# Kernel optimization log

Measured on AMD Instinct MI355X. Metric: run time of the kernel, lower is better.

Reference implementation:

```python
import jax, jax.numpy as jnp
import numpy as np

TAU_MEM = 0.005   # sinabs LIF tau_mem (in time-step units)
THR = 1.0         # default spike_threshold
BATCH = 16        # LIFSqueeze batch_size; leading dim is BATCH * T
BETA = 10.0       # surrogate gradient sharpness (sinabs SingleExponential default)


@jax.custom_vjp
def spike_fn(v):
    # MultiSpike: number of spikes = floor(v / thr), clipped at 0
    return jnp.floor(jnp.clip(v / THR, 0.0, None))

def _spike_fwd(v):
    return spike_fn(v), v

def _spike_bwd(v, g):
    # single-exponential surrogate gradient around threshold
    return (g * jnp.exp(-BETA * jnp.abs(v - THR)),)

spike_fn.defvjp(_spike_fwd, _spike_bwd)


def lif(x, spiking=True):
    """LIFSqueeze: x is (BATCH*T, ...); unfold time, scan LIF dynamics, refold."""
    alpha = jnp.exp(jnp.asarray(-1.0 / TAU_MEM, x.dtype))
    T = x.shape[0] // BATCH
    xt = jnp.swapaxes(x.reshape(BATCH, T, *x.shape[1:]), 0, 1)  # (T, B, ...)

    def step(v, xin):
        v = alpha * v + (1.0 - alpha) * xin  # norm_input=True: decay + scaled input
        if spiking:
            s = spike_fn(v)
            return v - s * THR, s            # membrane-subtract reset
        return v, v                          # spike_fn=None -> leaky integrator readout

    _, out = jax.lax.scan(step, jnp.zeros_like(xt[0]), xt)
    return jnp.swapaxes(out, 0, 1).reshape(x.shape)


def conv(x, w, stride, pad):
    return jax.lax.conv_general_dilated(
        x, w, (stride, stride), [(pad, pad), (pad, pad)],
        dimension_numbers=("NCHW", "OIHW", "NCHW"))


def maxpool2(x):
    return jax.lax.reduce_window(x, -jnp.inf, jax.lax.max,
                                 (1, 1, 2, 2), (1, 1, 2, 2), "VALID")


def setup_inputs() -> dict:
    key = jax.random.key(0)
    k = jax.random.split(key, 5)
    x = jax.random.normal(k[0], (1024, 2, 128, 128), jnp.float32)  # (B*T, C, H, W)
    w1 = jax.random.normal(k[1], (8, 2, 2, 2), jnp.float32) * (1.0 / np.sqrt(2 * 4))
    w2 = jax.random.normal(k[2], (8, 8, 3, 3), jnp.float32) * (1.0 / np.sqrt(8 * 9))
    w3 = jax.random.normal(k[3], (8, 8, 3, 3), jnp.float32) * (1.0 / np.sqrt(8 * 9))
    w_fc = jax.random.normal(k[4], (2, 512), jnp.float32) * (1.0 / np.sqrt(512))
    return {"x": x, "w1": w1, "w2": w2, "w3": w3, "w_fc": w_fc}


def reference(x, w1, w2, w3, w_fc):
    h = lif(conv(x, w1, 2, 0))        # (N, 8, 64, 64)
    h = maxpool2(h)                   # (N, 8, 32, 32)
    h = lif(conv(h, w2, 1, 1))
    h = maxpool2(h)                   # (N, 8, 16, 16)
    h = lif(conv(h, w3, 1, 1))
    h = maxpool2(h)                   # (N, 8, 8, 8)
    h = h.reshape(h.shape[0], -1)     # (N, 512)
    h = h @ w_fc.T                    # (N, 2)
    return lif(h, spiking=False)      # membrane-potential readout
```

## Files before the change

### kernel.cpp

```cpp
#include <hip/hip_runtime.h>
#include <cstddef>


__global__ __launch_bounds__(256) void k1_conv_pool(
    const float* __restrict__ x,
    const float* __restrict__ w1,
    float* __restrict__ out)
{
    int idx = blockIdx.x * 256 + threadIdx.x;
    int n  = idx >> 10;
    int py = (idx >> 5) & 31;
    int px = idx & 31;

    float w[64];
#pragma unroll
    for (int i = 0; i < 64; ++i) w[i] = w1[i];

    const float* xb = x + (size_t)n * (2 * 128 * 128);
    float p[2][4][4];
#pragma unroll
    for (int c = 0; c < 2; ++c)
#pragma unroll
        for (int r = 0; r < 4; ++r) {
            float4 v = *reinterpret_cast<const float4*>(
                xb + (c * 128 + 4 * py + r) * 128 + 4 * px);
            p[c][r][0] = v.x; p[c][r][1] = v.y; p[c][r][2] = v.z; p[c][r][3] = v.w;
        }

    float res[8];
#pragma unroll
    for (int co = 0; co < 8; ++co) res[co] = 0.f;

#pragma unroll
    for (int oy = 0; oy < 2; ++oy)
#pragma unroll
    for (int ox = 0; ox < 2; ++ox)
#pragma unroll
    for (int co = 0; co < 8; ++co) {
        float a = 0.f;
#pragma unroll
        for (int c = 0; c < 2; ++c)
#pragma unroll
        for (int kh = 0; kh < 2; ++kh)
#pragma unroll
        for (int kw = 0; kw < 2; ++kw)
            a += p[c][2 * oy + kh][2 * ox + kw] * w[((co * 2 + c) * 2 + kh) * 2 + kw];
        res[co] = fmaxf(res[co], floorf(fmaxf(a, 0.f)));
    }

    float* ob = out + (size_t)n * 8192 + py * 32 + px;
#pragma unroll
    for (int co = 0; co < 8; ++co) ob[co * 1024] = res[co];
}

__global__ __launch_bounds__(256) void k2_conv_pool(
    const float* __restrict__ in,
    const float* __restrict__ w2,
    float* __restrict__ out)
{
    __shared__ float tile[8][34][34];
    int n = blockIdx.x;
    int t = threadIdx.x;

    for (int i = t; i < 8 * 34 * 34; i += 256) (&tile[0][0][0])[i] = 0.f;
    __syncthreads();

    const float4* ib4 = reinterpret_cast<const float4*>(in + (size_t)n * 8192);
    for (int i4 = t; i4 < 2048; i4 += 256) {
        float4 v = ib4[i4];
        int ci = i4 >> 8, y = (i4 >> 3) & 31, x4 = (i4 & 7) << 2;
        tile[ci][y + 1][x4 + 1] = v.x;
        tile[ci][y + 1][x4 + 2] = v.y;
        tile[ci][y + 1][x4 + 3] = v.z;
        tile[ci][y + 1][x4 + 4] = v.w;
    }
    __syncthreads();

    int px = t & 15, py = t >> 4;
    float acc[8][2][2];
#pragma unroll
    for (int i = 0; i < 32; ++i) (&acc[0][0][0])[i] = 0.f;

    for (int ci = 0; ci < 8; ++ci) {
        float p[4][4];
#pragma unroll
        for (int r = 0; r < 4; ++r)
#pragma unroll
            for (int j = 0; j < 4; ++j)
                p[r][j] = tile[ci][2 * py + r][2 * px + j];
#pragma unroll
        for (int co = 0; co < 8; ++co) {
            const float* wp = w2 + (co * 8 + ci) * 9;
            float wv[9];
#pragma unroll
            for (int i = 0; i < 9; ++i) wv[i] = wp[i];
#pragma unroll
            for (int oy = 0; oy < 2; ++oy)
#pragma unroll
            for (int ox = 0; ox < 2; ++ox) {
                float a = acc[co][oy][ox];
#pragma unroll
                for (int kh = 0; kh < 3; ++kh)
#pragma unroll
                for (int kw = 0; kw < 3; ++kw)
                    a += p[oy + kh][ox + kw] * wv[kh * 3 + kw];
                acc[co][oy][ox] = a;
            }
        }
    }

    float* ob = out + (size_t)n * 2048;
#pragma unroll
    for (int co = 0; co < 8; ++co) {
        float m = 0.f;
#pragma unroll
        for (int oy = 0; oy < 2; ++oy)
#pragma unroll
        for (int ox = 0; ox < 2; ++ox)
            m = fmaxf(m, floorf(fmaxf(acc[co][oy][ox], 0.f)));
        ob[co * 256 + t] = m;
    }
}

__global__ __launch_bounds__(256) void k3_conv_pool_fc(
    const float* __restrict__ in,
    const float* __restrict__ w3,
    const float* __restrict__ wfc,
    float* __restrict__ out)
{
    __shared__ float tile[4][8][18][18];
    int t = threadIdx.x;

    for (int i = t; i < 4 * 8 * 18 * 18; i += 256) (&tile[0][0][0][0])[i] = 0.f;
    __syncthreads();

    const float4* ib4 = reinterpret_cast<const float4*>(in) + (size_t)blockIdx.x * 2048;
    for (int i4 = t; i4 < 2048; i4 += 256) {
        float4 v = ib4[i4];
        int sub = i4 >> 9, rem = i4 & 511;
        int ci = rem >> 6, y = (rem >> 2) & 15, x4 = (rem & 3) << 2;
        tile[sub][ci][y + 1][x4 + 1] = v.x;
        tile[sub][ci][y + 1][x4 + 2] = v.y;
        tile[sub][ci][y + 1][x4 + 3] = v.z;
        tile[sub][ci][y + 1][x4 + 4] = v.w;
    }
    __syncthreads();

    int sub = t >> 6;
    int l   = t & 63;
    int py = l >> 3, px = l & 7;

    float acc[8][2][2];
#pragma unroll
    for (int i = 0; i < 32; ++i) (&acc[0][0][0])[i] = 0.f;

    for (int ci = 0; ci < 8; ++ci) {
        float p[4][4];
#pragma unroll
        for (int r = 0; r < 4; ++r)
#pragma unroll
            for (int j = 0; j < 4; ++j)
                p[r][j] = tile[sub][ci][2 * py + r][2 * px + j];
#pragma unroll
        for (int co = 0; co < 8; ++co) {
            const float* wp = w3 + (co * 8 + ci) * 9;
            float wv[9];
#pragma unroll
            for (int i = 0; i < 9; ++i) wv[i] = wp[i];
#pragma unroll
            for (int oy = 0; oy < 2; ++oy)
#pragma unroll
            for (int ox = 0; ox < 2; ++ox) {
                float a = acc[co][oy][ox];
#pragma unroll
                for (int kh = 0; kh < 3; ++kh)
#pragma unroll
                for (int kw = 0; kw < 3; ++kw)
                    a += p[oy + kh][ox + kw] * wv[kh * 3 + kw];
                acc[co][oy][ox] = a;
            }
        }
    }

    float p0 = 0.f, p1 = 0.f;
#pragma unroll
    for (int co = 0; co < 8; ++co) {
        float m = 0.f;
#pragma unroll
        for (int oy = 0; oy < 2; ++oy)
#pragma unroll
        for (int ox = 0; ox < 2; ++ox)
            m = fmaxf(m, floorf(fmaxf(acc[co][oy][ox], 0.f)));
        int o = co * 64 + l;
        p0 += m * wfc[o];
        p1 += m * wfc[512 + o];
    }

#pragma unroll
    for (int off = 32; off > 0; off >>= 1) {
        p0 += __shfl_down(p0, off);
        p1 += __shfl_down(p1, off);
    }
    if (l == 0) {
        int n = blockIdx.x * 4 + sub;
        out[n * 2 + 0] = p0;
        out[n * 2 + 1] = p1;
    }
}

extern "C" void kernel_launch(void* const* d_in, const int* in_sizes, int n_in,
                              void* d_out, int out_size, void* d_ws, size_t ws_size,
                              hipStream_t stream) {
    const float* x   = (const float*)d_in[0];
    const float* w1  = (const float*)d_in[1];
    const float* w2  = (const float*)d_in[2];
    const float* w3  = (const float*)d_in[3];
    const float* wfc = (const float*)d_in[4];
    float* outp = (float*)d_out;

    float* h1 = (float*)d_ws;
    float* h2 = h1 + (size_t)1024 * 8192;

    k1_conv_pool<<<4096, 256, 0, stream>>>(x, w1, h1);
    k2_conv_pool<<<1024, 256, 0, stream>>>(h1, w2, h2);
    k3_conv_pool_fc<<<256, 256, 0, stream>>>(h2, w3, wfc, outp);
}
```

Baseline: 224.5 us.

## Fuse three conv-pool stages into a single per-sample kernel using LDS

Replaces three separate kernels with one kernel in which each block handles one sample. The conv1 and conv2 outputs are kept in shared-memory tiles, so the two intermediate buffers no longer make a round trip through global memory, and two launches go away. The third stage now splits output channels across the four waves, and a shared-memory reduction combines the FC partial sums. The trade-off is higher LDS use per block, which may lower occupancy, and a serialized load-then-compute phase inside each block.

```diff
diff --git a/kernel.cpp b/kernel.cpp
--- a/kernel.cpp
+++ b/kernel.cpp
@@ -2,209 +2,180 @@
 #include <cstddef>
 
 
-__global__ __launch_bounds__(256) void k1_conv_pool(
+__global__ __launch_bounds__(256, 4) void fused_snn(
     const float* __restrict__ x,
     const float* __restrict__ w1,
-    float* __restrict__ out)
-{
-    int idx = blockIdx.x * 256 + threadIdx.x;
-    int n  = idx >> 10;
-    int py = (idx >> 5) & 31;
-    int px = idx & 31;
-
-    float w[64];
-#pragma unroll
-    for (int i = 0; i < 64; ++i) w[i] = w1[i];
-
-    const float* xb = x + (size_t)n * (2 * 128 * 128);
-    float p[2][4][4];
-#pragma unroll
-    for (int c = 0; c < 2; ++c)
-#pragma unroll
-        for (int r = 0; r < 4; ++r) {
-            float4 v = *reinterpret_cast<const float4*>(
-                xb + (c * 128 + 4 * py + r) * 128 + 4 * px);
-            p[c][r][0] = v.x; p[c][r][1] = v.y; p[c][r][2] = v.z; p[c][r][3] = v.w;
-        }
-
-    float res[8];
-#pragma unroll
-    for (int co = 0; co < 8; ++co) res[co] = 0.f;
-
-#pragma unroll
-    for (int oy = 0; oy < 2; ++oy)
-#pragma unroll
-    for (int ox = 0; ox < 2; ++ox)
-#pragma unroll
-    for (int co = 0; co < 8; ++co) {
-        float a = 0.f;
-#pragma unroll
-        for (int c = 0; c < 2; ++c)
-#pragma unroll
-        for (int kh = 0; kh < 2; ++kh)
-#pragma unroll
-        for (int kw = 0; kw < 2; ++kw)
-            a += p[c][2 * oy + kh][2 * ox + kw] * w[((co * 2 + c) * 2 + kh) * 2 + kw];
-        res[co] = fmaxf(res[co], floorf(fmaxf(a, 0.f)));
-    }
-
-    float* ob = out + (size_t)n * 8192 + py * 32 + px;
-#pragma unroll
-    for (int co = 0; co < 8; ++co) ob[co * 1024] = res[co];
-}
-
-__global__ __launch_bounds__(256) void k2_conv_pool(
-    const float* __restrict__ in,
     const float* __restrict__ w2,
-    float* __restrict__ out)
-{
-    __shared__ float tile[8][34][34];
-    int n = blockIdx.x;
-    int t = threadIdx.x;
-
-    for (int i = t; i < 8 * 34 * 34; i += 256) (&tile[0][0][0])[i] = 0.f;
-    __syncthreads();
-
-    const float4* ib4 = reinterpret_cast<const float4*>(in + (size_t)n * 8192);
-    for (int i4 = t; i4 < 2048; i4 += 256) {
-        float4 v = ib4[i4];
-        int ci = i4 >> 8, y = (i4 >> 3) & 31, x4 = (i4 & 7) << 2;
-        tile[ci][y + 1][x4 + 1] = v.x;
-        tile[ci][y + 1][x4 + 2] = v.y;
-        tile[ci][y + 1][x4 + 3] = v.z;
-        tile[ci][y + 1][x4 + 4] = v.w;
-    }
-    __syncthreads();
-
-    int px = t & 15, py = t >> 4;
-    float acc[8][2][2];
-#pragma unroll
-    for (int i = 0; i < 32; ++i) (&acc[0][0][0])[i] = 0.f;
-
-    for (int ci = 0; ci < 8; ++ci) {
-        float p[4][4];
-#pragma unroll
-        for (int r = 0; r < 4; ++r)
-#pragma unroll
-            for (int j = 0; j < 4; ++j)
-                p[r][j] = tile[ci][2 * py + r][2 * px + j];
-#pragma unroll
-        for (int co = 0; co < 8; ++co) {
-            const float* wp = w2 + (co * 8 + ci) * 9;
-            float wv[9];
-#pragma unroll
-            for (int i = 0; i < 9; ++i) wv[i] = wp[i];
-#pragma unroll
-            for (int oy = 0; oy < 2; ++oy)
-#pragma unroll
-            for (int ox = 0; ox < 2; ++ox) {
-                float a = acc[co][oy][ox];
-#pragma unroll
-                for (int kh = 0; kh < 3; ++kh)
-#pragma unroll
-                for (int kw = 0; kw < 3; ++kw)
-                    a += p[oy + kh][ox + kw] * wv[kh * 3 + kw];
-                acc[co][oy][ox] = a;
-            }
-        }
-    }
-
-    float* ob = out + (size_t)n * 2048;
-#pragma unroll
-    for (int co = 0; co < 8; ++co) {
-        float m = 0.f;
-#pragma unroll
-        for (int oy = 0; oy < 2; ++oy)
-#pragma unroll
-        for (int ox = 0; ox < 2; ++ox)
-            m = fmaxf(m, floorf(fmaxf(acc[co][oy][ox], 0.f)));
-        ob[co * 256 + t] = m;
-    }
-}
-
-__global__ __launch_bounds__(256) void k3_conv_pool_fc(
-    const float* __restrict__ in,
     const float* __restrict__ w3,
     const float* __restrict__ wfc,
     float* __restrict__ out)
 {
-    __shared__ float tile[4][8][18][18];
-    int t = threadIdx.x;
+    __shared__ __align__(16) float t1[8][34][34];
+    __shared__ __align__(16) float t2[8][18][18];
+    __shared__ float red[8];
 
-    for (int i = t; i < 4 * 8 * 18 * 18; i += 256) (&tile[0][0][0][0])[i] = 0.f;
+    const int n = blockIdx.x;
+    const int t = threadIdx.x;
+
+    for (int i = t; i < 8 * 34 * 34; i += 256) (&t1[0][0][0])[i] = 0.f;
+    for (int i = t; i < 8 * 18 * 18; i += 256) (&t2[0][0][0])[i] = 0.f;
+
+    float wa[64];
+#pragma unroll
+    for (int i = 0; i < 64; ++i) wa[i] = w1[i];
     __syncthreads();
 
-    const float4* ib4 = reinterpret_cast<const float4*>(in) + (size_t)blockIdx.x * 2048;
-    for (int i4 = t; i4 < 2048; i4 += 256) {
-        float4 v = ib4[i4];
-        int sub = i4 >> 9, rem = i4 & 511;
-        int ci = rem >> 6, y = (rem >> 2) & 15, x4 = (rem & 3) << 2;
-        tile[sub][ci][y + 1][x4 + 1] = v.x;
-        tile[sub][ci][y + 1][x4 + 2] = v.y;
-        tile[sub][ci][y + 1][x4 + 3] = v.z;
-        tile[sub][ci][y + 1][x4 + 4] = v.w;
+    {
+        const float* xb = x + (size_t)n * (2 * 128 * 128);
+#pragma unroll 1
+        for (int k = 0; k < 4; ++k) {
+            int i = (k << 8) + t;
+            int py = i >> 5, px = i & 31;
+            float p[2][4][4];
+#pragma unroll
+            for (int c = 0; c < 2; ++c)
+#pragma unroll
+                for (int r = 0; r < 4; ++r) {
+                    float4 v = *reinterpret_cast<const float4*>(
+                        xb + (c * 128 + 4 * py + r) * 128 + 4 * px);
+                    p[c][r][0] = v.x; p[c][r][1] = v.y; p[c][r][2] = v.z; p[c][r][3] = v.w;
+                }
+#pragma unroll
+            for (int co = 0; co < 8; ++co) {
+                float m = 0.f;
+#pragma unroll
+                for (int oy = 0; oy < 2; ++oy)
+#pragma unroll
+                for (int ox = 0; ox < 2; ++ox) {
+                    float a = 0.f;
+#pragma unroll
+                    for (int c = 0; c < 2; ++c)
+#pragma unroll
+                    for (int kh = 0; kh < 2; ++kh)
+#pragma unroll
+                    for (int kw = 0; kw < 2; ++kw)
+                        a += p[c][2 * oy + kh][2 * ox + kw] * wa[((co * 2 + c) * 2 + kh) * 2 + kw];
+                    m = fmaxf(m, floorf(fmaxf(a, 0.f)));
+                }
+                t1[co][py + 1][px + 1] = m;
+            }
+        }
     }
     __syncthreads();
 
-    int sub = t >> 6;
-    int l   = t & 63;
-    int py = l >> 3, px = l & 7;
+    {
+        const int py = t >> 4, px = t & 15;
+        float acc[8][2][2];
+#pragma unroll
+        for (int i = 0; i < 32; ++i) (&acc[0][0][0])[i] = 0.f;
 
-    float acc[8][2][2];
+#pragma unroll 1
+        for (int ci = 0; ci < 8; ++ci) {
+            float p[4][4];
 #pragma unroll
-    for (int i = 0; i < 32; ++i) (&acc[0][0][0])[i] = 0.f;
-
-    for (int ci = 0; ci < 8; ++ci) {
-        float p[4][4];
+            for (int r = 0; r < 4; ++r) {
+                const float2* row = reinterpret_cast<const float2*>(&t1[ci][2 * py + r][0]);
+                float2 a = row[px], b = row[px + 1];
+                p[r][0] = a.x; p[r][1] = a.y; p[r][2] = b.x; p[r][3] = b.y;
+            }
 #pragma unroll
-        for (int r = 0; r < 4; ++r)
+            for (int co = 0; co < 8; ++co) {
+                const float* wp = w2 + (co * 8 + ci) * 9;
+                float wv[9];
 #pragma unroll
-            for (int j = 0; j < 4; ++j)
-                p[r][j] = tile[sub][ci][2 * py + r][2 * px + j];
+                for (int i = 0; i < 9; ++i) wv[i] = wp[i];
+#pragma unroll
+                for (int oy = 0; oy < 2; ++oy)
+#pragma unroll
+                for (int ox = 0; ox < 2; ++ox) {
+                    float a = acc[co][oy][ox];
+#pragma unroll
+                    for (int kh = 0; kh < 3; ++kh)
+#pragma unroll
+                    for (int kw = 0; kw < 3; ++kw)
+                        a += p[oy + kh][ox + kw] * wv[kh * 3 + kw];
+                    acc[co][oy][ox] = a;
+                }
+            }
+        }
 #pragma unroll
         for (int co = 0; co < 8; ++co) {
-            const float* wp = w3 + (co * 8 + ci) * 9;
-            float wv[9];
-#pragma unroll
-            for (int i = 0; i < 9; ++i) wv[i] = wp[i];
+            float m = 0.f;
 #pragma unroll
             for (int oy = 0; oy < 2; ++oy)
 #pragma unroll
-            for (int ox = 0; ox < 2; ++ox) {
-                float a = acc[co][oy][ox];
+            for (int ox = 0; ox < 2; ++ox)
+                m = fmaxf(m, floorf(fmaxf(acc[co][oy][ox], 0.f)));
+            t2[co][py + 1][px + 1] = m;
+        }
+    }
+    __syncthreads();
+
+    {
+        const int co2 = __builtin_amdgcn_readfirstlane(t >> 6);
+        const int l = t & 63;
+        const int py = l >> 3, px = l & 7;
+
+        float acc[2][2][2];
 #pragma unroll
-                for (int kh = 0; kh < 3; ++kh)
+        for (int i = 0; i < 8; ++i) (&acc[0][0][0])[i] = 0.f;
+
+#pragma unroll 1
+        for (int ci = 0; ci < 8; ++ci) {
+            float p[4][4];
 #pragma unroll
-                for (int kw = 0; kw < 3; ++kw)
-                    a += p[oy + kh][ox + kw] * wv[kh * 3 + kw];
-                acc[co][oy][ox] = a;
+            for (int r = 0; r < 4; ++r) {
+                const float2* row = reinterpret_cast<const float2*>(&t2[ci][2 * py + r][0]);
+                float2 a = row[px], b = row[px + 1];
+                p[r][0] = a.x; p[r][1] = a.y; p[r][2] = b.x; p[r][3] = b.y;
+            }
+#pragma unroll
+            for (int cc = 0; cc < 2; ++cc) {
+                const float* wp = w3 + ((2 * co2 + cc) * 8 + ci) * 9;
+                float wv[9];
+#pragma unroll
+                for (int i = 0; i < 9; ++i) wv[i] = wp[i];
+#pragma unroll
+                for (int oy = 0; oy < 2; ++oy)
+#pragma unroll
+                for (int ox = 0; ox < 2; ++ox) {
+                    float a = acc[cc][oy][ox];
+#pragma unroll
+                    for (int kh = 0; kh < 3; ++kh)
+#pragma unroll
+                    for (int kw = 0; kw < 3; ++kw)
+                        a += p[oy + kh][ox + kw] * wv[kh * 3 + kw];
+                    acc[cc][oy][ox] = a;
+                }
             }
         }
-    }
 
-    float p0 = 0.f, p1 = 0.f;
+        float p0 = 0.f, p1 = 0.f;
 #pragma unroll
-    for (int co = 0; co < 8; ++co) {
-        float m = 0.f;
+        for (int cc = 0; cc < 2; ++cc) {
+            float m = 0.f;
 #pragma unroll
-        for (int oy = 0; oy < 2; ++oy)
+            for (int oy = 0; oy < 2; ++oy)
 #pragma unroll
-        for (int ox = 0; ox < 2; ++ox)
-            m = fmaxf(m, floorf(fmaxf(acc[co][oy][ox], 0.f)));
-        int o = co * 64 + l;
-        p0 += m * wfc[o];
-        p1 += m * wfc[512 + o];
-    }
+            for (int ox = 0; ox < 2; ++ox)
+                m = fmaxf(m, floorf(fmaxf(acc[cc][oy][ox], 0.f)));
+            int o = (2 * co2 + cc) * 64 + l;
+            p0 += m * wfc[o];
+            p1 += m * wfc[512 + o];
+        }
 
 #pragma unroll
-    for (int off = 32; off > 0; off >>= 1) {
-        p0 += __shfl_down(p0, off);
-        p1 += __shfl_down(p1, off);
+        for (int off = 32; off > 0; off >>= 1) {
+            p0 += __shfl_down(p0, off);
+            p1 += __shfl_down(p1, off);
+        }
+        if (l == 0) { red[co2 * 2 + 0] = p0; red[co2 * 2 + 1] = p1; }
     }
-    if (l == 0) {
-        int n = blockIdx.x * 4 + sub;
-        out[n * 2 + 0] = p0;
-        out[n * 2 + 1] = p1;
+    __syncthreads();
+
+    if (t == 0) {
+        out[n * 2 + 0] = red[0] + red[2] + red[4] + red[6];
+        out[n * 2 + 1] = red[1] + red[3] + red[5] + red[7];
     }
 }
 
@@ -218,10 +189,5 @@
     const float* wfc = (const float*)d_in[4];
     float* outp = (float*)d_out;
 
-    float* h1 = (float*)d_ws;
-    float* h2 = h1 + (size_t)1024 * 8192;
-
-    k1_conv_pool<<<4096, 256, 0, stream>>>(x, w1, h1);
-    k2_conv_pool<<<1024, 256, 0, stream>>>(h1, w2, h2);
-    k3_conv_pool_fc<<<256, 256, 0, stream>>>(h2, w3, wfc, outp);
+    fused_snn<<<1024, 256, 0, stream>>>(x, w1, w2, w3, wfc, outp);
 }
```

After: 209.8 us. 6.5% less time.
